# Performance work log

Measured on AMD Instinct MI355X. Metric: run time of the kernel, lower is better.

Reference implementation:

```python
import jax, jax.numpy as jnp
import numpy as np

ALPHA = 0.2  # LeakyReLU negative slope


def setup_inputs() -> dict:
    key = jax.random.key(0)
    k1, k2, k3, k4 = jax.random.split(key, 4)
    B, Cin, Cout, N, T, Kt = 8, 64, 64, 2048, 13, 3
    L = T - Kt + 1  # 11, must equal `length`
    x = jax.random.normal(k1, (B, Cin, N, T), dtype=jnp.float32)
    w0 = jax.random.normal(k2, (Cout, Cin, 1, Kt), dtype=jnp.float32) * 0.05
    b0 = jax.random.normal(k3, (Cout,), dtype=jnp.float32) * 0.05
    w1 = jax.random.normal(k4, (Cout * L,), dtype=jnp.float32) * 0.05
    return {"x": x, "w0": w0, "b0": b0, "w1": w1}


def reference(x, w0, b0, w1):
    # conv0: Conv2d(in,out,(1,Kt)), VALID padding -> [B, Cout, N, L]
    h = jax.lax.conv_general_dilated(
        x, w0, window_strides=(1, 1), padding='VALID',
        dimension_numbers=('NCHW', 'OIHW', 'NCHW')) + b0[None, :, None, None]
    B, C, N, L = h.shape
    # permute(0,1,3,2).view(B, C*L, N) then 1x1 Conv1d (no bias) == contraction over (c,l)
    # NOTE: original module uses conv1 for BOTH f_1 and f_2 (conv2 unused), so f_1 == f_2.
    f = jnp.einsum('bcnl,cl->bn', h, w1.reshape(C, L))  # [B, N]
    logits = f[:, :, None] + f[:, None, :]              # [B, N, N]
    lrelu = jnp.where(logits >= 0, logits, ALPHA * logits)
    attention = jax.nn.softmax(lrelu, axis=-1)          # softmax over last (column) dim
    attention = jnp.swapaxes(attention, -1, -2)         # [B, N, N] transposed
    # h_prime[b,c,q,l] = sum_n h[b,c,n,l] * attention[b,n,q]
    h_prime = jnp.einsum('bcnl,bnq->bcql', h, attention)
    return h_prime, attention
```

## Files before the change

kernel.cpp:

```cpp
#include <hip/hip_runtime.h>

#define BB 8
#define CIN 64
#define COUT 64
#define NN 2048
#define TT 13
#define KTT 3
#define LL 11
#define CL 704
#define HP_SIZE 11534336LL

#define WS_TAB_OFF 65568ULL
#define WS_W0PK_OFF 327712ULL
#define WS_APAN_OFF 352288ULL

typedef _Float16 f16;
typedef __attribute__((ext_vector_type(8))) _Float16 f16x8;
typedef __attribute__((ext_vector_type(2))) _Float16 f16x2;
typedef __attribute__((ext_vector_type(4))) float f32x4;

__device__ __forceinline__ unsigned int pk16(float a, float b) {
  f16 ha = (f16)a, hb = (f16)b;
  unsigned short ua = __builtin_bit_cast(unsigned short, ha);
  unsigned short ub = __builtin_bit_cast(unsigned short, hb);
  return (unsigned int)ua | ((unsigned int)ub << 16);
}
__device__ __forceinline__ f16x2 as_h2(unsigned int u) {
  return __builtin_bit_cast(f16x2, u);
}

__global__ __launch_bounds__(256) void k_pack(const float* __restrict__ w0,
                                              unsigned int* __restrict__ w0pk_g) {
  int tid = blockIdx.x * 256 + threadIdx.x;
  int c = tid & 63, r = tid >> 6;
  int kt = r % 3, cip = r / 3;
  float ev = w0[c * 192 + cip * 6 + kt];
  float od = w0[c * 192 + cip * 6 + 3 + kt];
  w0pk_g[r * 64 + c] = pk16(ev, od);
}

__global__ __launch_bounds__(512, 4) void k_conv(
    const float* __restrict__ x, const unsigned int* __restrict__ w0pk_g,
    const float* __restrict__ b0, const float* __restrict__ w1,
    f16* __restrict__ Apan, float* __restrict__ f) {
  __shared__ unsigned int w0pk[96 * 64];
  __shared__ unsigned int xspk[32 * 8 * 16];
  __shared__ f16 As[704 * 10];
  const int tid = threadIdx.x;
  const int b = blockIdx.x >> 8;
  const int n0 = (blockIdx.x & 255) << 3;

#pragma unroll
  for (int i = 0; i < 12; ++i) w0pk[i * 512 + tid] = w0pk_g[i * 512 + tid];

#pragma unroll
  for (int i = 0; i < 7; ++i) {
    int task = i * 512 + tid;
    if (task < 3328) {
      int cip = task / 104, rem = task - cip * 104;
      long long base = (long long)(b * 64 + 2 * cip) * 26624 + n0 * 13 + rem;
      float ev = x[base];
      float od = x[base + 26624];
      int n = rem / 13, t = rem - n * 13;
      xspk[(cip * 8 + n) * 16 + t] = pk16(ev, od);
    }
  }
  __syncthreads();

  const int c = tid & 63, w = tid >> 6;
  float acc[11];
  const float bias = b0[c];
#pragma unroll
  for (int l = 0; l < 11; ++l) acc[l] = bias;

  for (int cip = 0; cip < 32; ++cip) {
    const unsigned int* xr = &xspk[(cip * 8 + w) * 16];
    uint4 xa = *(const uint4*)xr;
    uint4 xb = *(const uint4*)(xr + 4);
    uint4 xc = *(const uint4*)(xr + 8);
    unsigned int x13[13] = {xa.x, xa.y, xa.z, xa.w, xb.x, xb.y, xb.z, xb.w,
                            xc.x, xc.y, xc.z, xc.w, xr[12]};
    f16x2 wk0 = as_h2(w0pk[(cip * 3 + 0) * 64 + c]);
    f16x2 wk1 = as_h2(w0pk[(cip * 3 + 1) * 64 + c]);
    f16x2 wk2 = as_h2(w0pk[(cip * 3 + 2) * 64 + c]);
#pragma unroll
    for (int l = 0; l < 11; ++l) {
      acc[l] = __builtin_amdgcn_fdot2(as_h2(x13[l]), wk0, acc[l], false);
      acc[l] = __builtin_amdgcn_fdot2(as_h2(x13[l + 1]), wk1, acc[l], false);
      acc[l] = __builtin_amdgcn_fdot2(as_h2(x13[l + 2]), wk2, acc[l], false);
    }
  }

  float p = 0.f;
#pragma unroll
  for (int l = 0; l < 11; ++l) p = fmaf(acc[l], w1[c * 11 + l], p);
#pragma unroll
  for (int off = 32; off; off >>= 1) p += __shfl_xor(p, off, 64);
  if (c == 0) f[b * 2048 + n0 + w] = p;

#pragma unroll
  for (int l = 0; l < 11; ++l) As[(c * 11 + l) * 10 + w] = (f16)acc[l];
  __syncthreads();

  const int ks = n0 >> 5, kgrp = (n0 >> 3) & 3;
  const unsigned int* As32 = (const unsigned int*)As;
#pragma unroll
  for (int i = 0; i < 2; ++i) {
    int m = i * 512 + tid;
    if (m < 704) {
      uint4 v;
      v.x = As32[m * 5 + 0];
      v.y = As32[m * 5 + 1];
      v.z = As32[m * 5 + 2];
      v.w = As32[m * 5 + 3];
      int mt = m >> 6, fr = (m >> 4) & 3, r16 = m & 15;
      long long base = ((long long)(b * 11 + mt) * 64 + ks) * 2048 +
                       fr * 512 + (kgrp * 16 + r16) * 8;
      *(uint4*)&Apan[base] = v;
    }
  }
}

__global__ __launch_bounds__(256) void k_maxf(const float* __restrict__ f,
                                              float* __restrict__ maxf) {
  const int b = blockIdx.x, tid = threadIdx.x;
  float m = -1e30f;
  for (int i = tid; i < 2048; i += 256) m = fmaxf(m, f[b * 2048 + i]);
#pragma unroll
  for (int off = 32; off; off >>= 1) m = fmaxf(m, __shfl_xor(m, off, 64));
  __shared__ float red[4];
  if ((tid & 63) == 0) red[tid >> 6] = m;
  __syncthreads();
  if (tid == 0) maxf[b] = fmaxf(fmaxf(red[0], red[1]), fmaxf(red[2], red[3]));
}

__global__ __launch_bounds__(256) void k_rowsum(const float* __restrict__ f,
                                                const float* __restrict__ maxf,
                                                float4* __restrict__ tab4) {
  __shared__ float fs[2048];
  const int b = blockIdx.x >> 9;
  const int q0 = (blockIdx.x & 511) << 2;
  const int tid = threadIdx.x;
#pragma unroll
  for (int i = 0; i < 8; ++i) fs[i * 256 + tid] = f[b * 2048 + i * 256 + tid];
  __syncthreads();
  const int lane = tid & 63, wid = tid >> 6;
  const int q = q0 + wid;
  const float fq = fs[q];
  const float mb = maxf[b];
  float t = fq + mb;
  const float m = t >= 0.f ? t : 0.2f * t;
  float sum = 0.f;
  for (int j = lane; j < 2048; j += 64) {
    float v = fq + fs[j];
    v = v >= 0.f ? v : 0.2f * v;
    sum += __expf(v - m);
  }
#pragma unroll
  for (int off = 32; off; off >>= 1) sum += __shfl_xor(sum, off, 64);
  if (lane == 0) {
    float rq = 1.0f / sum;
    float En = __expf(fq - mb);
    float E2 = __expf(0.2f * fq);
    float Rq = t >= 0.f ? rq : rq * __expf(0.8f * t);
    float Sq = rq * __expf(0.2f * fq - m);
    tab4[b * 2048 + q] = make_float4(En, E2, Rq, Sq);
  }
}

__global__ __launch_bounds__(256, 4) void k_gemm(const f16* __restrict__ Apan,
                                                 const float4* __restrict__ tab4,
                                                 float* __restrict__ att,
                                                 float* __restrict__ out) {
  __shared__ __align__(16) float2 Etab[2048];

  const int p = blockIdx.x;
  const int g = p % 88, qt = p / 88;
  const int b = g / 11, mt = g % 11;

  const int tid = threadIdx.x;
  const int qw = tid >> 6, lane = tid & 63;
  const int l15 = lane & 15, l4 = lane >> 4;

  const f16* Ab = Apan + ((long long)(b * 11 + mt) * 64) * 2048 + lane * 8;
  const float4* tb = tab4 + (long long)b * NN;

#pragma unroll
  for (int i = 0; i < 8; ++i) {
    int idx = i * 256 + tid;
    float4 v = tb[idx];
    Etab[idx] = make_float2(v.x, v.y);
  }
  const int q0 = qt * 128 + qw * 32 + l15;
  float Rq0, Sq0, Rq1, Sq1;
  { float4 t4 = tb[q0];      Rq0 = t4.z; Sq0 = t4.w; }
  { float4 t4 = tb[q0 + 16]; Rq1 = t4.z; Sq1 = t4.w; }
  __syncthreads();

  f32x4 acc[4][2];
#pragma unroll
  for (int fr = 0; fr < 4; ++fr)
#pragma unroll
    for (int nf = 0; nf < 2; ++nf) acc[fr][nf] = (f32x4){0.f, 0.f, 0.f, 0.f};

  f16x8 c0 = *(const f16x8*)(Ab);
  f16x8 c1 = *(const f16x8*)(Ab + 512);
  f16x8 c2 = *(const f16x8*)(Ab + 1024);
  f16x8 c3 = *(const f16x8*)(Ab + 1536);

  for (int ks = 0; ks < 64; ++ks) {
    f16x8 n0 = c0, n1 = c1, n2 = c2, n3 = c3;
    if (ks < 63) {
      const f16* at = Ab + (ks + 1) * 2048;
      n0 = *(const f16x8*)(at);
      n1 = *(const f16x8*)(at + 512);
      n2 = *(const f16x8*)(at + 1024);
      n3 = *(const f16x8*)(at + 1536);
    }
    const int nb = ks * 32 + l4 * 8;
    const float4* ep = (const float4*)&Etab[nb];
    float4 e0 = ep[0], e1 = ep[1], e2 = ep[2], e3 = ep[3];
    float En[8] = {e0.x, e0.z, e1.x, e1.z, e2.x, e2.z, e3.x, e3.z};
    float E2[8] = {e0.y, e0.w, e1.y, e1.w, e2.y, e2.w, e3.y, e3.w};
    const bool owned = ((ks * 11) >> 6) == mt;
    const long long abase = ((long long)(b * 2048 + nb)) * 2048 + q0;

#pragma unroll
    for (int nf = 0; nf < 2; ++nf) {
      const float Rq = nf == 0 ? Rq0 : Rq1;
      const float Sq = nf == 0 ? Sq0 : Sq1;
      f16x8 bv;
      float vf[8];
#pragma unroll
      for (int u = 0; u < 8; ++u) {
        float val = fmaxf(En[u] * Rq, E2[u] * Sq);
        vf[u] = val;
        bv[u] = (f16)val;
      }
      if (owned) {
        float* ap = att + abase + nf * 16;
#pragma unroll
        for (int u = 0; u < 8; ++u) ap[(long long)u * 2048] = vf[u];
      }
      acc[0][nf] = __builtin_amdgcn_mfma_f32_16x16x32_f16(c0, bv, acc[0][nf], 0, 0, 0);
      acc[1][nf] = __builtin_amdgcn_mfma_f32_16x16x32_f16(c1, bv, acc[1][nf], 0, 0, 0);
      acc[2][nf] = __builtin_amdgcn_mfma_f32_16x16x32_f16(c2, bv, acc[2][nf], 0, 0, 0);
      acc[3][nf] = __builtin_amdgcn_mfma_f32_16x16x32_f16(c3, bv, acc[3][nf], 0, 0, 0);
    }
    c0 = n0; c1 = n1; c2 = n2; c3 = n3;
  }

  float* ob = out + (long long)b * COUT * NN * LL;
#pragma unroll
  for (int fr = 0; fr < 4; ++fr) {
#pragma unroll
    for (int r = 0; r < 4; ++r) {
      int m = mt * 64 + fr * 16 + l4 * 4 + r;
      int c = m / 11, l2 = m - c * 11;
      float* orow = ob + (long long)c * NN * LL + l2;
#pragma unroll
      for (int nf = 0; nf < 2; ++nf) {
        int q = q0 + nf * 16;
        orow[(long long)q * LL] = acc[fr][nf][r];
      }
    }
  }
}

extern "C" void kernel_launch(void* const* d_in, const int* in_sizes, int n_in,
                              void* d_out, int out_size, void* d_ws, size_t ws_size,
                              hipStream_t stream) {
  const float* x  = (const float*)d_in[0];
  const float* w0 = (const float*)d_in[1];
  const float* b0 = (const float*)d_in[2];
  const float* w1 = (const float*)d_in[3];

  float* fbuf = (float*)d_ws;
  float* maxf = fbuf + BB * NN;
  float4* tab4 = (float4*)((char*)d_ws + WS_TAB_OFF);
  unsigned int* w0pk_g = (unsigned int*)((char*)d_ws + WS_W0PK_OFF);
  f16* Apan = (f16*)((char*)d_ws + WS_APAN_OFF);

  float* hp  = (float*)d_out;
  float* att = hp + HP_SIZE;

  k_pack<<<dim3(24), dim3(256), 0, stream>>>(w0, w0pk_g);
  k_conv<<<dim3(BB * 256), dim3(512), 0, stream>>>(x, w0pk_g, b0, w1, Apan, fbuf);
  k_maxf<<<dim3(BB), dim3(256), 0, stream>>>(fbuf, maxf);
  k_rowsum<<<dim3(BB * 512), dim3(256), 0, stream>>>(fbuf, maxf, tab4);
  k_gemm<<<dim3(88 * 16), dim3(256), 0, stream>>>(Apan, tab4, att, hp);
}
```

Before: 169.9 us.

## Split attention build into separate kernel and stream precomputed f16 B panel into GEMM

A new k_build kernel computes the attention matrix once, writes it in fp32, and also packs an f16 copy into a workspace panel laid out for MFMA B-operand loads. The GEMM then streams that panel instead of recomputing exp-based values 11 times per tile and doing strided attention stores. Its block order is also remapped so that blocks sharing a batch and q-tile run close together, improving cache reuse. This adds a 64MB f16 write plus reads from it, and keeps a recompute fallback path for when the workspace is too small.

```diff
diff --git a/kernel.cpp b/kernel.cpp
--- a/kernel.cpp
+++ b/kernel.cpp
@@ -13,6 +13,8 @@
 #define WS_TAB_OFF 65568ULL
 #define WS_W0PK_OFF 327712ULL
 #define WS_APAN_OFF 352288ULL
+#define WS_BPAN_OFF 23420960ULL
+#define WS_NEED (23420960ULL + 67108864ULL)
 
 typedef _Float16 f16;
 typedef __attribute__((ext_vector_type(8))) _Float16 f16x8;
@@ -168,23 +170,134 @@
   }
 }
 
+template <int WITH_BPAN>
+__global__ __launch_bounds__(256) void k_build(const float4* __restrict__ tab4,
+                                               float* __restrict__ att,
+                                               f16* __restrict__ Bpan) {
+  const int b = blockIdx.x >> 6, ks = blockIdx.x & 63;
+  const int tid = threadIdx.x;
+  __shared__ float2 Etb[32];
+  if (tid < 32) {
+    float4 v = tab4[b * 2048 + ks * 32 + tid];
+    Etb[tid] = make_float2(v.x, v.y);
+  }
+  __syncthreads();
+  float En[32], E2[32];
+#pragma unroll
+  for (int i = 0; i < 32; ++i) { En[i] = Etb[i].x; E2[i] = Etb[i].y; }
+
+  float* ab = att + ((long long)(b * 2048 + ks * 32)) * 2048;
+  f16* bp = Bpan + (((long long)(b * 64 + ks)) * 4) * 2048 * 8;
+
+#pragma unroll
+  for (int j = 0; j < 8; ++j) {
+    const int q = tid + j * 256;
+    float4 t4 = tab4[b * 2048 + q];
+    const float Rq = t4.z, Sq = t4.w;
+#pragma unroll
+    for (int kg = 0; kg < 4; ++kg) {
+      float v[8];
+#pragma unroll
+      for (int kk = 0; kk < 8; ++kk) {
+        int n = kg * 8 + kk;
+        float val = fmaxf(En[n] * Rq, E2[n] * Sq);
+        v[kk] = val;
+        ab[(long long)n * 2048 + q] = val;
+      }
+      if (WITH_BPAN) {
+        uint4 w;
+        w.x = pk16(v[0], v[1]);
+        w.y = pk16(v[2], v[3]);
+        w.z = pk16(v[4], v[5]);
+        w.w = pk16(v[6], v[7]);
+        *(uint4*)&bp[((long long)kg * 2048 + q) * 8] = w;
+      }
+    }
+  }
+}
+
 __global__ __launch_bounds__(256, 4) void k_gemm(const f16* __restrict__ Apan,
-                                                 const float4* __restrict__ tab4,
-                                                 float* __restrict__ att,
+                                                 const f16* __restrict__ Bpan,
                                                  float* __restrict__ out) {
+  const int p = blockIdx.x;
+  const int x = p & 7, r = p >> 3;
+  const int mt = r % 11, Gh = r / 11;
+  const int G = Gh * 8 + x;
+  const int b = G >> 4, qt = G & 15;
+
+  const int tid = threadIdx.x;
+  const int qw = tid >> 6, lane = tid & 63;
+  const int l15 = lane & 15, l4 = lane >> 4;
+  const int q0 = qt * 128 + qw * 32 + l15;
+
+  const f16* Ab = Apan + ((long long)(b * 11 + mt) * 64) * 2048 + lane * 8;
+  const f16* Bb = Bpan + (((long long)(b * 64) * 4 + l4) * 2048 + q0) * 8;
+
+  f32x4 acc[4][2];
+#pragma unroll
+  for (int fr = 0; fr < 4; ++fr)
+#pragma unroll
+    for (int nf = 0; nf < 2; ++nf) acc[fr][nf] = (f32x4){0.f, 0.f, 0.f, 0.f};
+
+  f16x8 ca0 = *(const f16x8*)(Ab);
+  f16x8 ca1 = *(const f16x8*)(Ab + 512);
+  f16x8 ca2 = *(const f16x8*)(Ab + 1024);
+  f16x8 ca3 = *(const f16x8*)(Ab + 1536);
+  f16x8 cb0 = *(const f16x8*)(Bb);
+  f16x8 cb1 = *(const f16x8*)(Bb + 128);
+
+  for (int ks = 0; ks < 64; ++ks) {
+    f16x8 na0 = ca0, na1 = ca1, na2 = ca2, na3 = ca3, nb0 = cb0, nb1 = cb1;
+    if (ks < 63) {
+      const f16* at = Ab + (ks + 1) * 2048;
+      const f16* bt = Bb + (long long)(ks + 1) * 65536;
+      na0 = *(const f16x8*)(at);
+      na1 = *(const f16x8*)(at + 512);
+      na2 = *(const f16x8*)(at + 1024);
+      na3 = *(const f16x8*)(at + 1536);
+      nb0 = *(const f16x8*)(bt);
+      nb1 = *(const f16x8*)(bt + 128);
+    }
+#pragma unroll
+    for (int nf = 0; nf < 2; ++nf) {
+      f16x8 bv = nf == 0 ? cb0 : cb1;
+      acc[0][nf] = __builtin_amdgcn_mfma_f32_16x16x32_f16(ca0, bv, acc[0][nf], 0, 0, 0);
+      acc[1][nf] = __builtin_amdgcn_mfma_f32_16x16x32_f16(ca1, bv, acc[1][nf], 0, 0, 0);
+      acc[2][nf] = __builtin_amdgcn_mfma_f32_16x16x32_f16(ca2, bv, acc[2][nf], 0, 0, 0);
+      acc[3][nf] = __builtin_amdgcn_mfma_f32_16x16x32_f16(ca3, bv, acc[3][nf], 0, 0, 0);
+    }
+    ca0 = na0; ca1 = na1; ca2 = na2; ca3 = na3; cb0 = nb0; cb1 = nb1;
+  }
+
+  float* ob = out + (long long)b * COUT * NN * LL;
+#pragma unroll
+  for (int fr = 0; fr < 4; ++fr) {
+#pragma unroll
+    for (int rr = 0; rr < 4; ++rr) {
+      int m = mt * 64 + fr * 16 + l4 * 4 + rr;
+      int c = m / 11, l2 = m - c * 11;
+      float* orow = ob + (long long)c * NN * LL + l2;
+#pragma unroll
+      for (int nf = 0; nf < 2; ++nf) {
+        int q = q0 + nf * 16;
+        orow[(long long)q * LL] = acc[fr][nf][rr];
+      }
+    }
+  }
+}
+
+__global__ __launch_bounds__(256, 4) void k_gemm_fb(const f16* __restrict__ Apan,
+                                                    const float4* __restrict__ tab4,
+                                                    float* __restrict__ out) {
   __shared__ __align__(16) float2 Etab[2048];
-
   const int p = blockIdx.x;
   const int g = p % 88, qt = p / 88;
   const int b = g / 11, mt = g % 11;
-
   const int tid = threadIdx.x;
   const int qw = tid >> 6, lane = tid & 63;
   const int l15 = lane & 15, l4 = lane >> 4;
-
   const f16* Ab = Apan + ((long long)(b * 11 + mt) * 64) * 2048 + lane * 8;
   const float4* tb = tab4 + (long long)b * NN;
-
 #pragma unroll
   for (int i = 0; i < 8; ++i) {
     int idx = i * 256 + tid;
@@ -196,18 +309,15 @@
   { float4 t4 = tb[q0];      Rq0 = t4.z; Sq0 = t4.w; }
   { float4 t4 = tb[q0 + 16]; Rq1 = t4.z; Sq1 = t4.w; }
   __syncthreads();
-
   f32x4 acc[4][2];
 #pragma unroll
   for (int fr = 0; fr < 4; ++fr)
 #pragma unroll
     for (int nf = 0; nf < 2; ++nf) acc[fr][nf] = (f32x4){0.f, 0.f, 0.f, 0.f};
-
   f16x8 c0 = *(const f16x8*)(Ab);
   f16x8 c1 = *(const f16x8*)(Ab + 512);
   f16x8 c2 = *(const f16x8*)(Ab + 1024);
   f16x8 c3 = *(const f16x8*)(Ab + 1536);
-
   for (int ks = 0; ks < 64; ++ks) {
     f16x8 n0 = c0, n1 = c1, n2 = c2, n3 = c3;
     if (ks < 63) {
@@ -222,26 +332,13 @@
     float4 e0 = ep[0], e1 = ep[1], e2 = ep[2], e3 = ep[3];
     float En[8] = {e0.x, e0.z, e1.x, e1.z, e2.x, e2.z, e3.x, e3.z};
     float E2[8] = {e0.y, e0.w, e1.y, e1.w, e2.y, e2.w, e3.y, e3.w};
-    const bool owned = ((ks * 11) >> 6) == mt;
-    const long long abase = ((long long)(b * 2048 + nb)) * 2048 + q0;
-
 #pragma unroll
     for (int nf = 0; nf < 2; ++nf) {
       const float Rq = nf == 0 ? Rq0 : Rq1;
       const float Sq = nf == 0 ? Sq0 : Sq1;
       f16x8 bv;
-      float vf[8];
-#pragma unroll
-      for (int u = 0; u < 8; ++u) {
-        float val = fmaxf(En[u] * Rq, E2[u] * Sq);
-        vf[u] = val;
-        bv[u] = (f16)val;
-      }
-      if (owned) {
-        float* ap = att + abase + nf * 16;
-#pragma unroll
-        for (int u = 0; u < 8; ++u) ap[(long long)u * 2048] = vf[u];
-      }
+#pragma unroll
+      for (int u = 0; u < 8; ++u) bv[u] = (f16)fmaxf(En[u] * Rq, E2[u] * Sq);
       acc[0][nf] = __builtin_amdgcn_mfma_f32_16x16x32_f16(c0, bv, acc[0][nf], 0, 0, 0);
       acc[1][nf] = __builtin_amdgcn_mfma_f32_16x16x32_f16(c1, bv, acc[1][nf], 0, 0, 0);
       acc[2][nf] = __builtin_amdgcn_mfma_f32_16x16x32_f16(c2, bv, acc[2][nf], 0, 0, 0);
@@ -249,20 +346,17 @@
     }
     c0 = n0; c1 = n1; c2 = n2; c3 = n3;
   }
-
   float* ob = out + (long long)b * COUT * NN * LL;
 #pragma unroll
   for (int fr = 0; fr < 4; ++fr) {
 #pragma unroll
-    for (int r = 0; r < 4; ++r) {
-      int m = mt * 64 + fr * 16 + l4 * 4 + r;
+    for (int rr = 0; rr < 4; ++rr) {
+      int m = mt * 64 + fr * 16 + l4 * 4 + rr;
       int c = m / 11, l2 = m - c * 11;
       float* orow = ob + (long long)c * NN * LL + l2;
 #pragma unroll
-      for (int nf = 0; nf < 2; ++nf) {
-        int q = q0 + nf * 16;
-        orow[(long long)q * LL] = acc[fr][nf][r];
-      }
+      for (int nf = 0; nf < 2; ++nf)
+        orow[(long long)(q0 + nf * 16) * LL] = acc[fr][nf][rr];
     }
   }
 }
@@ -280,6 +374,7 @@
   float4* tab4 = (float4*)((char*)d_ws + WS_TAB_OFF);
   unsigned int* w0pk_g = (unsigned int*)((char*)d_ws + WS_W0PK_OFF);
   f16* Apan = (f16*)((char*)d_ws + WS_APAN_OFF);
+  f16* Bpan = (f16*)((char*)d_ws + WS_BPAN_OFF);
 
   float* hp  = (float*)d_out;
   float* att = hp + HP_SIZE;
@@ -288,5 +383,11 @@
   k_conv<<<dim3(BB * 256), dim3(512), 0, stream>>>(x, w0pk_g, b0, w1, Apan, fbuf);
   k_maxf<<<dim3(BB), dim3(256), 0, stream>>>(fbuf, maxf);
   k_rowsum<<<dim3(BB * 512), dim3(256), 0, stream>>>(fbuf, maxf, tab4);
-  k_gemm<<<dim3(88 * 16), dim3(256), 0, stream>>>(Apan, tab4, att, hp);
-}
+  if (ws_size >= WS_NEED) {
+    k_build<1><<<dim3(BB * 64), dim3(256), 0, stream>>>(tab4, att, Bpan);
+    k_gemm<<<dim3(1408), dim3(256), 0, stream>>>(Apan, Bpan, hp);
+  } else {
+    k_build<0><<<dim3(BB * 64), dim3(256), 0, stream>>>(tab4, att, Bpan);
+    k_gemm_fb<<<dim3(88 * 16), dim3(256), 0, stream>>>(Apan, tab4, hp);
+  }
+}
```

Result: slower. 210.3 us (+23.8%).
